# Kernel optimization log

Measured on AMD Instinct MI355X. Metric: run time of the kernel, lower is better.

## Reference

```python
import jax, jax.numpy as jnp
import numpy as np

N_DIMS = 4          # Euclidean GA with metric [1,1,1,1]
NUM_BLADES = 1 << N_DIMS  # 16 blades
B, N_IN, UNITS = 128, 512, 512


def _cayley_table(n_dims: int) -> np.ndarray:
    """Geometric-product Cayley table C[i,j,k] for Euclidean metric (+1,...,+1).

    Blades are indexed by bitmasks over the n basis vectors; e_A * e_B = sign * e_{A^B},
    where sign counts transpositions in the canonical reordering.
    """
    num = 1 << n_dims
    C = np.zeros((num, num, num), dtype=np.float32)
    for a in range(num):
        for b in range(num):
            t, swaps = a >> 1, 0
            while t:
                swaps += bin(t & b).count("1")
                t >>= 1
            C[a, b, a ^ b] = -1.0 if (swaps & 1) else 1.0
    return C


def setup_inputs() -> dict:
    key = jax.random.key(0)
    k1, k2, k3 = jax.random.split(key, 3)
    x = jax.random.normal(k1, (B, N_IN, NUM_BLADES), dtype=jnp.float32)
    w = jax.random.normal(k2, (UNITS, N_IN, NUM_BLADES), dtype=jnp.float32)
    b = jax.random.normal(k3, (UNITS, NUM_BLADES), dtype=jnp.float32)
    cayley = jnp.asarray(_cayley_table(N_DIMS))
    return {"x": x, "w": w, "b": b, "cayley": cayley}


def reference(x, w, b, cayley):
    # geom_prod(x[..., None, n, i], w[u, n, j])[..., u, n, k], summed over n, plus bias:
    # out[b,u,k] = sum_{n,i,j} x[b,n,i] * cayley[i,j,k] * w[u,n,j] + b[u,k]
    out = jnp.einsum("bni,ijk,unj->buk", x, cayley, w)
    return out + b
```

## Files before the change

### kernel.cpp

```cpp
#include <hip/hip_runtime.h>
#include <stdint.h>

typedef unsigned short ushort_t;
typedef __attribute__((ext_vector_type(8))) short short8v;
typedef __attribute__((ext_vector_type(4))) float f32x4;

#define NSPLIT 8

#define AT_ELEMS (16u * 128u * 512u)
#define WT_ELEMS (16u * 512u * 512u)
#define P_OFF_BYTES ((size_t)(AT_ELEMS + WT_ELEMS) * 2u)
#define P_ELEMS ((size_t)NSPLIT * 16 * 128 * 512)
#define WS_NEEDED (P_OFF_BYTES + P_ELEMS * 4u)

__host__ __device__ constexpr int ga_sign_i(int a, int b) {
  int t = a >> 1, sw = 0;
  while (t) {
    int x = t & b;
    while (x) { sw += x & 1; x >>= 1; }
    t >>= 1;
  }
  return (sw & 1) ? -1 : 1;
}

struct SignTab { int s[16][16]; };
constexpr SignTab make_tab() {
  SignTab t{};
  for (int i = 0; i < 16; i++)
    for (int j = 0; j < 16; j++) t.s[i][j] = ga_sign_i(i, j);
  return t;
}
constexpr SignTab STAB = make_tab();

__device__ __forceinline__ ushort_t f2bf(float f) {
  unsigned u = __float_as_uint(f);
  u = (u + 0x7FFFu + ((u >> 16) & 1u)) >> 16;
  return (ushort_t)u;
}

__device__ __forceinline__ short8v neg_bf16x8(short8v v) {
  const short m = (short)0x8000;
  return v ^ (short8v){m, m, m, m, m, m, m, m};
}

#define PREP_XT (128 * 512)
#define PREP_TOT (PREP_XT + 512 * 512)

__global__ __launch_bounds__(256) void prep_kernel(const float* __restrict__ x,
                                                   const float* __restrict__ w,
                                                   ushort_t* __restrict__ At,
                                                   ushort_t* __restrict__ Wt) {
  int tid = blockIdx.x * 256 + threadIdx.x;
  if (tid < PREP_XT) {
    int n = tid & 511, b = tid >> 9;
    const float4* xp = (const float4*)(x + (size_t)tid * 16);
    float v[16];
#pragma unroll
    for (int qq = 0; qq < 4; qq++) {
      float4 t = xp[qq];
      v[qq * 4 + 0] = t.x; v[qq * 4 + 1] = t.y; v[qq * 4 + 2] = t.z; v[qq * 4 + 3] = t.w;
    }
#pragma unroll
    for (int j = 0; j < 16; j++)
      At[((size_t)(j * 128 + b)) * 512 + n] = f2bf(v[j]);
  } else {
    int t = tid - PREP_XT;
    int n = t & 511, u = t >> 9;
    const float4* wp = (const float4*)(w + (size_t)t * 16);
    float v[16];
#pragma unroll
    for (int qq = 0; qq < 4; qq++) {
      float4 tt = wp[qq];
      v[qq * 4 + 0] = tt.x; v[qq * 4 + 1] = tt.y; v[qq * 4 + 2] = tt.z; v[qq * 4 + 3] = tt.w;
    }
#pragma unroll
    for (int j = 0; j < 16; j++)
      Wt[((size_t)(j * 512 + u)) * 512 + n] = f2bf(v[j]);
  }
}

template <int W>
__device__ __forceinline__ void compute_chunk(const char* sm, int lbx,
                                              f32x4 (&acc)[4][2][2]) {
#pragma unroll
  for (int jh = 0; jh < 4; jh++) {
    const int ig = jh ^ W;
    short8v av[4][2], bv[4][2];
#pragma unroll
    for (int il = 0; il < 4; il++)
#pragma unroll
      for (int f = 0; f < 2; f++)
        av[il][f] = *(const short8v*)(sm + ((ig * 4 + il) * 32 + f * 16) * 64 + lbx);
#pragma unroll
    for (int jl = 0; jl < 4; jl++)
#pragma unroll
      for (int g = 0; g < 2; g++)
        bv[jl][g] = *(const short8v*)(sm + 32768 + ((jh * 4 + jl) * 32 + g * 16) * 64 + lbx);
#pragma unroll
    for (int kl = 0; kl < 4; kl++) {
#pragma unroll
      for (int jl = 0; jl < 4; jl++) {
        const int il = jl ^ kl;
        const int i = ig * 4 + il;
        const int j = jh * 4 + jl;
        short8v a0 = av[il][0], a1 = av[il][1];
        if (STAB.s[i][j] < 0) { a0 = neg_bf16x8(a0); a1 = neg_bf16x8(a1); }
        acc[kl][0][0] = __builtin_amdgcn_mfma_f32_16x16x32_bf16(a0, bv[jl][0], acc[kl][0][0], 0, 0, 0);
        acc[kl][0][1] = __builtin_amdgcn_mfma_f32_16x16x32_bf16(a0, bv[jl][1], acc[kl][0][1], 0, 0, 0);
        acc[kl][1][0] = __builtin_amdgcn_mfma_f32_16x16x32_bf16(a1, bv[jl][0], acc[kl][1][0], 0, 0, 0);
        acc[kl][1][1] = __builtin_amdgcn_mfma_f32_16x16x32_bf16(a1, bv[jl][1], acc[kl][1][1], 0, 0, 0);
      }
    }
  }
}

__global__ __launch_bounds__(256, 2) void gemm_kernel(const ushort_t* __restrict__ At,
                                                      const ushort_t* __restrict__ Wt,
                                                      float* __restrict__ P) {
  __shared__ __align__(16) ushort_t smem[32768];

  const int ut = blockIdx.x;
  const int bt = blockIdx.y;
  const int sp = blockIdx.z;
  const int u0 = ut * 32, b0 = bt * 32, n0 = sp * 64;

  const int wv = threadIdx.x >> 6;
  const int lane = threadIdx.x & 63;

  int offX[8], offW[8];
#pragma unroll
  for (int it = 0; it < 8; it++) {
    int slot = it * 256 + wv * 64 + lane;
    int r = slot >> 2, p = slot & 3;
    int q = p ^ (r & 3) ^ ((r >> 2) & 3);
    offX[it] = ((r >> 5) * 128 + (r & 31)) * 512 + q * 8;
    offW[it] = ((r >> 5) * 512 + (r & 31)) * 512 + q * 8;
  }
  const ushort_t* Ax = At + (size_t)b0 * 512 + n0;
  const ushort_t* Wx = Wt + (size_t)u0 * 512 + n0;

  const int la = lane & 15, q = lane >> 4;
  const int lbx = la * 64 + (q ^ (la & 3) ^ ((la >> 2) & 3)) * 16;

  f32x4 acc[4][2][2];
#pragma unroll
  for (int a = 0; a < 4; a++)
#pragma unroll
    for (int f = 0; f < 2; f++)
#pragma unroll
      for (int g = 0; g < 2; g++) acc[a][f][g] = (f32x4){0.f, 0.f, 0.f, 0.f};

  const char* sm = (const char*)smem;

#pragma unroll 1
  for (int kt = 0; kt < 2; kt++) {
#pragma unroll
    for (int it = 0; it < 8; it++)
      __builtin_amdgcn_global_load_lds(
          (const __attribute__((address_space(1))) unsigned int*)(Ax + offX[it] + kt * 32),
          (__attribute__((address_space(3))) unsigned int*)(&smem[(it * 256 + wv * 64) * 8]),
          16, 0, 0);
#pragma unroll
    for (int it = 0; it < 8; it++)
      __builtin_amdgcn_global_load_lds(
          (const __attribute__((address_space(1))) unsigned int*)(Wx + offW[it] + kt * 32),
          (__attribute__((address_space(3))) unsigned int*)(&smem[16384 + (it * 256 + wv * 64) * 8]),
          16, 0, 0);
    __syncthreads();
    switch (wv) {
      case 0: compute_chunk<0>(sm, lbx, acc); break;
      case 1: compute_chunk<1>(sm, lbx, acc); break;
      case 2: compute_chunk<2>(sm, lbx, acc); break;
      default: compute_chunk<3>(sm, lbx, acc); break;
    }
    __syncthreads();
  }

  float* Pb = P + (size_t)sp * 16 * 128 * 512;
#pragma unroll
  for (int kl = 0; kl < 4; kl++) {
    int k = wv * 4 + kl;
#pragma unroll
    for (int f = 0; f < 2; f++)
#pragma unroll
      for (int g = 0; g < 2; g++)
#pragma unroll
        for (int r2 = 0; r2 < 4; r2++) {
          int row = b0 + f * 16 + q * 4 + r2;
          int col = u0 + g * 16 + la;
          Pb[((size_t)(k * 128 + row)) * 512 + col] = acc[kl][f][g][r2];
        }
  }
}

__global__ __launch_bounds__(256) void reduce_kernel(const float* __restrict__ P,
                                                     const float* __restrict__ bias,
                                                     float* __restrict__ out) {
  int t = blockIdx.x * 256 + threadIdx.x;
  int u = t & 511;
  int b = t >> 9;
  float acc[16];
#pragma unroll
  for (int k = 0; k < 16; k++) acc[k] = bias[u * 16 + k];
  for (int s = 0; s < NSPLIT; s++) {
#pragma unroll
    for (int k = 0; k < 16; k++)
      acc[k] += P[((size_t)(s * 16 + k) * 128 + b) * 512 + u];
  }
  float* op = out + ((size_t)(b * 512 + u)) * 16;
#pragma unroll
  for (int qq = 0; qq < 4; qq++)
    ((float4*)op)[qq] = make_float4(acc[qq * 4 + 0], acc[qq * 4 + 1],
                                    acc[qq * 4 + 2], acc[qq * 4 + 3]);
}

__global__ __launch_bounds__(256) void naive_kernel(const float* __restrict__ x,
                                                    const float* __restrict__ w,
                                                    const float* __restrict__ bias,
                                                    float* __restrict__ out) {
  int t = blockIdx.x * 256 + threadIdx.x;
  if (t >= 128 * 512 * 16) return;
  int k = t & 15;
  int u = (t >> 4) & 511;
  int b = t >> 13;
  float sgn[16];
#pragma unroll
  for (int i = 0; i < 16; i++) sgn[i] = (float)ga_sign_i(i, i ^ k);
  float acc = bias[u * 16 + k];
  for (int n = 0; n < 512; n++) {
    const float* xp = x + ((size_t)(b * 512 + n)) * 16;
    const float* wp = w + ((size_t)(u * 512 + n)) * 16;
#pragma unroll
    for (int i = 0; i < 16; i++)
      acc += xp[i] * sgn[i] * wp[i ^ k];
  }
  out[t] = acc;
}

extern "C" void kernel_launch(void* const* d_in, const int* in_sizes, int n_in,
                              void* d_out, int out_size, void* d_ws, size_t ws_size,
                              hipStream_t stream) {
  const float* x    = (const float*)d_in[0];
  const float* w    = (const float*)d_in[1];
  const float* bias = (const float*)d_in[2];
  float* out = (float*)d_out;

  if (ws_size >= WS_NEEDED && d_ws != nullptr) {
    ushort_t* At = (ushort_t*)d_ws;
    ushort_t* Wt = At + AT_ELEMS;
    float* P = (float*)((char*)d_ws + P_OFF_BYTES);

    prep_kernel<<<PREP_TOT / 256, 256, 0, stream>>>(x, w, At, Wt);
    gemm_kernel<<<dim3(16, 4, NSPLIT), 256, 0, stream>>>(At, Wt, P);
    reduce_kernel<<<256, 256, 0, stream>>>(P, bias, out);
  } else {
    naive_kernel<<<(128 * 512 * 16) / 256, 256, 0, stream>>>(x, w, bias, out);
  }
}
```

Baseline: 102.3 us.

## Retile GA GEMM to 16-row batch tiles with fewer K splits and coalesced prep

The GEMM tile becomes 16 batch rows by 32 units with a 128-deep K slice per block, and the K split drops from 8 to 4. This halves the partial-sum buffer that the reduce kernel reads and writes. Each wave now precomputes the negated A fragments once per chunk instead of negating them per MFMA. The prep kernel is rewritten so each thread packs 8 consecutive n values into one 16-byte store, instead of issuing 16 scattered 2-byte stores. In exchange the prep loads become strided, each block does less MFMA work per shared-memory load, and the grid is reshaped.

```diff
diff --git a/kernel.cpp b/kernel.cpp
--- a/kernel.cpp
+++ b/kernel.cpp
@@ -5,7 +5,7 @@
 typedef __attribute__((ext_vector_type(8))) short short8v;
 typedef __attribute__((ext_vector_type(4))) float f32x4;
 
-#define NSPLIT 8
+#define NSPLIT 4
 
 #define AT_ELEMS (16u * 128u * 512u)
 #define WT_ELEMS (16u * 512u * 512u)
@@ -43,8 +43,8 @@
   return v ^ (short8v){m, m, m, m, m, m, m, m};
 }
 
-#define PREP_XT (128 * 512)
-#define PREP_TOT (PREP_XT + 512 * 512)
+#define PREP_XT (16 * 128 * 64)
+#define PREP_TOT (PREP_XT + 16 * 512 * 64)
 
 __global__ __launch_bounds__(256) void prep_kernel(const float* __restrict__ x,
                                                    const float* __restrict__ w,
@@ -52,50 +52,44 @@
                                                    ushort_t* __restrict__ Wt) {
   int tid = blockIdx.x * 256 + threadIdx.x;
   if (tid < PREP_XT) {
-    int n = tid & 511, b = tid >> 9;
-    const float4* xp = (const float4*)(x + (size_t)tid * 16);
-    float v[16];
-#pragma unroll
-    for (int qq = 0; qq < 4; qq++) {
-      float4 t = xp[qq];
-      v[qq * 4 + 0] = t.x; v[qq * 4 + 1] = t.y; v[qq * 4 + 2] = t.z; v[qq * 4 + 3] = t.w;
-    }
-#pragma unroll
-    for (int j = 0; j < 16; j++)
-      At[((size_t)(j * 128 + b)) * 512 + n] = f2bf(v[j]);
+    int n8 = tid & 63;
+    int bj = tid >> 6;
+    int b = bj & 127, j = bj >> 7;
+    ushort_t o[8];
+#pragma unroll
+    for (int r = 0; r < 8; r++)
+      o[r] = f2bf(x[((size_t)(b * 512 + n8 * 8 + r)) * 16 + j]);
+    *(uint4*)(At + ((size_t)(j * 128 + b)) * 512 + n8 * 8) = *(const uint4*)o;
   } else {
     int t = tid - PREP_XT;
-    int n = t & 511, u = t >> 9;
-    const float4* wp = (const float4*)(w + (size_t)t * 16);
-    float v[16];
-#pragma unroll
-    for (int qq = 0; qq < 4; qq++) {
-      float4 tt = wp[qq];
-      v[qq * 4 + 0] = tt.x; v[qq * 4 + 1] = tt.y; v[qq * 4 + 2] = tt.z; v[qq * 4 + 3] = tt.w;
-    }
-#pragma unroll
-    for (int j = 0; j < 16; j++)
-      Wt[((size_t)(j * 512 + u)) * 512 + n] = f2bf(v[j]);
+    int n8 = t & 63;
+    int uj = t >> 6;
+    int u = uj & 511, j = uj >> 9;
+    ushort_t o[8];
+#pragma unroll
+    for (int r = 0; r < 8; r++)
+      o[r] = f2bf(w[((size_t)(u * 512 + n8 * 8 + r)) * 16 + j]);
+    *(uint4*)(Wt + ((size_t)(j * 512 + u)) * 512 + n8 * 8) = *(const uint4*)o;
   }
 }
 
 template <int W>
 __device__ __forceinline__ void compute_chunk(const char* sm, int lbx,
-                                              f32x4 (&acc)[4][2][2]) {
+                                              f32x4 (&acc)[4][2]) {
 #pragma unroll
   for (int jh = 0; jh < 4; jh++) {
     const int ig = jh ^ W;
-    short8v av[4][2], bv[4][2];
-#pragma unroll
-    for (int il = 0; il < 4; il++)
-#pragma unroll
-      for (int f = 0; f < 2; f++)
-        av[il][f] = *(const short8v*)(sm + ((ig * 4 + il) * 32 + f * 16) * 64 + lbx);
+    short8v av[4], avn[4], bv[4][2];
+#pragma unroll
+    for (int il = 0; il < 4; il++) {
+      av[il] = *(const short8v*)(sm + (ig * 4 + il) * 1024 + lbx);
+      avn[il] = neg_bf16x8(av[il]);
+    }
 #pragma unroll
     for (int jl = 0; jl < 4; jl++)
 #pragma unroll
       for (int g = 0; g < 2; g++)
-        bv[jl][g] = *(const short8v*)(sm + 32768 + ((jh * 4 + jl) * 32 + g * 16) * 64 + lbx);
+        bv[jl][g] = *(const short8v*)(sm + 16384 + (jh * 4 + jl) * 2048 + g * 1024 + lbx);
 #pragma unroll
     for (int kl = 0; kl < 4; kl++) {
 #pragma unroll
@@ -103,12 +97,9 @@
         const int il = jl ^ kl;
         const int i = ig * 4 + il;
         const int j = jh * 4 + jl;
-        short8v a0 = av[il][0], a1 = av[il][1];
-        if (STAB.s[i][j] < 0) { a0 = neg_bf16x8(a0); a1 = neg_bf16x8(a1); }
-        acc[kl][0][0] = __builtin_amdgcn_mfma_f32_16x16x32_bf16(a0, bv[jl][0], acc[kl][0][0], 0, 0, 0);
-        acc[kl][0][1] = __builtin_amdgcn_mfma_f32_16x16x32_bf16(a0, bv[jl][1], acc[kl][0][1], 0, 0, 0);
-        acc[kl][1][0] = __builtin_amdgcn_mfma_f32_16x16x32_bf16(a1, bv[jl][0], acc[kl][1][0], 0, 0, 0);
-        acc[kl][1][1] = __builtin_amdgcn_mfma_f32_16x16x32_bf16(a1, bv[jl][1], acc[kl][1][1], 0, 0, 0);
+        const short8v a = (STAB.s[i][j] < 0) ? avn[il] : av[il];
+        acc[kl][0] = __builtin_amdgcn_mfma_f32_16x16x32_bf16(a, bv[jl][0], acc[kl][0], 0, 0, 0);
+        acc[kl][1] = __builtin_amdgcn_mfma_f32_16x16x32_bf16(a, bv[jl][1], acc[kl][1], 0, 0, 0);
       }
     }
   }
@@ -117,23 +108,29 @@
 __global__ __launch_bounds__(256, 2) void gemm_kernel(const ushort_t* __restrict__ At,
                                                       const ushort_t* __restrict__ Wt,
                                                       float* __restrict__ P) {
-  __shared__ __align__(16) ushort_t smem[32768];
+  __shared__ __align__(16) ushort_t smem[24576];
 
   const int ut = blockIdx.x;
   const int bt = blockIdx.y;
   const int sp = blockIdx.z;
-  const int u0 = ut * 32, b0 = bt * 32, n0 = sp * 64;
+  const int u0 = ut * 32, b0 = bt * 16, n0 = sp * 128;
 
   const int wv = threadIdx.x >> 6;
   const int lane = threadIdx.x & 63;
 
-  int offX[8], offW[8];
+  int offX[4], offW[8];
+#pragma unroll
+  for (int it = 0; it < 4; it++) {
+    int slot = it * 256 + wv * 64 + lane;
+    int r = slot >> 2, p = slot & 3;
+    int q = p ^ (r & 3) ^ ((r >> 2) & 3);
+    offX[it] = ((r >> 4) * 128 + (r & 15)) * 512 + q * 8;
+  }
 #pragma unroll
   for (int it = 0; it < 8; it++) {
     int slot = it * 256 + wv * 64 + lane;
     int r = slot >> 2, p = slot & 3;
     int q = p ^ (r & 3) ^ ((r >> 2) & 3);
-    offX[it] = ((r >> 5) * 128 + (r & 31)) * 512 + q * 8;
     offW[it] = ((r >> 5) * 512 + (r & 31)) * 512 + q * 8;
   }
   const ushort_t* Ax = At + (size_t)b0 * 512 + n0;
@@ -142,20 +139,18 @@
   const int la = lane & 15, q = lane >> 4;
   const int lbx = la * 64 + (q ^ (la & 3) ^ ((la >> 2) & 3)) * 16;
 
-  f32x4 acc[4][2][2];
+  f32x4 acc[4][2];
 #pragma unroll
   for (int a = 0; a < 4; a++)
 #pragma unroll
-    for (int f = 0; f < 2; f++)
-#pragma unroll
-      for (int g = 0; g < 2; g++) acc[a][f][g] = (f32x4){0.f, 0.f, 0.f, 0.f};
+    for (int g = 0; g < 2; g++) acc[a][g] = (f32x4){0.f, 0.f, 0.f, 0.f};
 
   const char* sm = (const char*)smem;
 
 #pragma unroll 1
-  for (int kt = 0; kt < 2; kt++) {
-#pragma unroll
-    for (int it = 0; it < 8; it++)
+  for (int kt = 0; kt < 4; kt++) {
+#pragma unroll
+    for (int it = 0; it < 4; it++)
       __builtin_amdgcn_global_load_lds(
           (const __attribute__((address_space(1))) unsigned int*)(Ax + offX[it] + kt * 32),
           (__attribute__((address_space(3))) unsigned int*)(&smem[(it * 256 + wv * 64) * 8]),
@@ -164,7 +159,7 @@
     for (int it = 0; it < 8; it++)
       __builtin_amdgcn_global_load_lds(
           (const __attribute__((address_space(1))) unsigned int*)(Wx + offW[it] + kt * 32),
-          (__attribute__((address_space(3))) unsigned int*)(&smem[16384 + (it * 256 + wv * 64) * 8]),
+          (__attribute__((address_space(3))) unsigned int*)(&smem[8192 + (it * 256 + wv * 64) * 8]),
           16, 0, 0);
     __syncthreads();
     switch (wv) {
@@ -181,15 +176,13 @@
   for (int kl = 0; kl < 4; kl++) {
     int k = wv * 4 + kl;
 #pragma unroll
-    for (int f = 0; f < 2; f++)
-#pragma unroll
-      for (int g = 0; g < 2; g++)
-#pragma unroll
-        for (int r2 = 0; r2 < 4; r2++) {
-          int row = b0 + f * 16 + q * 4 + r2;
-          int col = u0 + g * 16 + la;
-          Pb[((size_t)(k * 128 + row)) * 512 + col] = acc[kl][f][g][r2];
-        }
+    for (int g = 0; g < 2; g++)
+#pragma unroll
+      for (int r2 = 0; r2 < 4; r2++) {
+        int row = b0 + q * 4 + r2;
+        int col = u0 + g * 16 + la;
+        Pb[((size_t)(k * 128 + row)) * 512 + col] = acc[kl][g][r2];
+      }
   }
 }
 
@@ -251,7 +244,7 @@
     float* P = (float*)((char*)d_ws + P_OFF_BYTES);
 
     prep_kernel<<<PREP_TOT / 256, 256, 0, stream>>>(x, w, At, Wt);
-    gemm_kernel<<<dim3(16, 4, NSPLIT), 256, 0, stream>>>(At, Wt, P);
+    gemm_kernel<<<dim3(16, 8, NSPLIT), 256, 0, stream>>>(At, Wt, P);
     reduce_kernel<<<256, 256, 0, stream>>>(P, bias, out);
   } else {
     naive_kernel<<<(128 * 512 * 16) / 256, 256, 0, stream>>>(x, w, bias, out);
```

After: 107.5 us. 5.1% more time.

## Replace split-K partials and reduce kernel with in-block wave reduction

Applied to the files above, without the earlier changes.

Drops the split-K decomposition that wrote fp32 partials to workspace and the separate reduce kernel. Each block now owns a 16x16 (b,u) tile with all 16 output blades. Each wave covers a quarter of the n range and the four waves are summed through shared memory with the bias add fused in. This removes a kernel launch and the large partial-buffer traffic. In exchange it uses 128KB of LDS per block, so only one block fits per CU. The grid also shrinks to 256 blocks and the K loop becomes serial with no overlap between loads and compute.

```diff
diff --git a/kernel.cpp b/kernel.cpp
--- a/kernel.cpp
+++ b/kernel.cpp
@@ -5,13 +5,9 @@
 typedef __attribute__((ext_vector_type(8))) short short8v;
 typedef __attribute__((ext_vector_type(4))) float f32x4;
 
-#define NSPLIT 8
-
 #define AT_ELEMS (16u * 128u * 512u)
 #define WT_ELEMS (16u * 512u * 512u)
-#define P_OFF_BYTES ((size_t)(AT_ELEMS + WT_ELEMS) * 2u)
-#define P_ELEMS ((size_t)NSPLIT * 16 * 128 * 512)
-#define WS_NEEDED (P_OFF_BYTES + P_ELEMS * 4u)
+#define WS_NEEDED ((size_t)(AT_ELEMS + WT_ELEMS) * 2u)
 
 __host__ __device__ constexpr int ga_sign_i(int a, int b) {
   int t = a >> 1, sw = 0;
@@ -79,139 +75,101 @@
   }
 }
 
-template <int W>
-__device__ __forceinline__ void compute_chunk(const char* sm, int lbx,
-                                              f32x4 (&acc)[4][2][2]) {
-#pragma unroll
-  for (int jh = 0; jh < 4; jh++) {
-    const int ig = jh ^ W;
-    short8v av[4][2], bv[4][2];
-#pragma unroll
-    for (int il = 0; il < 4; il++)
-#pragma unroll
-      for (int f = 0; f < 2; f++)
-        av[il][f] = *(const short8v*)(sm + ((ig * 4 + il) * 32 + f * 16) * 64 + lbx);
-#pragma unroll
-    for (int jl = 0; jl < 4; jl++)
-#pragma unroll
-      for (int g = 0; g < 2; g++)
-        bv[jl][g] = *(const short8v*)(sm + 32768 + ((jh * 4 + jl) * 32 + g * 16) * 64 + lbx);
-#pragma unroll
-    for (int kl = 0; kl < 4; kl++) {
-#pragma unroll
-      for (int jl = 0; jl < 4; jl++) {
-        const int il = jl ^ kl;
-        const int i = ig * 4 + il;
-        const int j = jh * 4 + jl;
-        short8v a0 = av[il][0], a1 = av[il][1];
-        if (STAB.s[i][j] < 0) { a0 = neg_bf16x8(a0); a1 = neg_bf16x8(a1); }
-        acc[kl][0][0] = __builtin_amdgcn_mfma_f32_16x16x32_bf16(a0, bv[jl][0], acc[kl][0][0], 0, 0, 0);
-        acc[kl][0][1] = __builtin_amdgcn_mfma_f32_16x16x32_bf16(a0, bv[jl][1], acc[kl][0][1], 0, 0, 0);
-        acc[kl][1][0] = __builtin_amdgcn_mfma_f32_16x16x32_bf16(a1, bv[jl][0], acc[kl][1][0], 0, 0, 0);
-        acc[kl][1][1] = __builtin_amdgcn_mfma_f32_16x16x32_bf16(a1, bv[jl][1], acc[kl][1][1], 0, 0, 0);
-      }
-    }
-  }
-}
-
-__global__ __launch_bounds__(256, 2) void gemm_kernel(const ushort_t* __restrict__ At,
+__global__ __launch_bounds__(256, 1) void gemm_kernel(const ushort_t* __restrict__ At,
                                                       const ushort_t* __restrict__ Wt,
-                                                      float* __restrict__ P) {
-  __shared__ __align__(16) ushort_t smem[32768];
+                                                      const float* __restrict__ bias,
+                                                      float* __restrict__ out) {
+  __shared__ __align__(16) ushort_t smem[65536];
 
   const int ut = blockIdx.x;
   const int bt = blockIdx.y;
-  const int sp = blockIdx.z;
-  const int u0 = ut * 32, b0 = bt * 32, n0 = sp * 64;
-
-  const int wv = threadIdx.x >> 6;
-  const int lane = threadIdx.x & 63;
-
-  int offX[8], offW[8];
-#pragma unroll
-  for (int it = 0; it < 8; it++) {
-    int slot = it * 256 + wv * 64 + lane;
-    int r = slot >> 2, p = slot & 3;
-    int q = p ^ (r & 3) ^ ((r >> 2) & 3);
-    offX[it] = ((r >> 5) * 128 + (r & 31)) * 512 + q * 8;
-    offW[it] = ((r >> 5) * 512 + (r & 31)) * 512 + q * 8;
-  }
-  const ushort_t* Ax = At + (size_t)b0 * 512 + n0;
-  const ushort_t* Wx = Wt + (size_t)u0 * 512 + n0;
-
+  const int u0 = ut * 16, b0 = bt * 16;
+
+  const int tid = threadIdx.x;
+  const int wv = tid >> 6, lane = tid & 63;
   const int la = lane & 15, q = lane >> 4;
-  const int lbx = la * 64 + (q ^ (la & 3) ^ ((la >> 2) & 3)) * 16;
-
-  f32x4 acc[4][2][2];
-#pragma unroll
-  for (int a = 0; a < 4; a++)
-#pragma unroll
-    for (int f = 0; f < 2; f++)
-#pragma unroll
-      for (int g = 0; g < 2; g++) acc[a][f][g] = (f32x4){0.f, 0.f, 0.f, 0.f};
+
+  const int srow = tid >> 4;
+  const int sps = tid & 15;
+  const int sp = sps ^ (srow & 7);
+  const int sc = sp >> 2, sq = sp & 3;
+
+  const ushort_t* AxB = At + (size_t)(b0 + srow) * 512 + sc * 32 + sq * 8;
+  const ushort_t* WxB = Wt + (size_t)(u0 + srow) * 512 + sc * 32 + sq * 8;
+
+  const int pr = wv * 4 + q;
+  const int lbx = la * 256 + ((pr ^ (la & 7)) * 16);
+
+  f32x4 acc[16];
+#pragma unroll
+  for (int k = 0; k < 16; k++) acc[k] = (f32x4){0.f, 0.f, 0.f, 0.f};
 
   const char* sm = (const char*)smem;
 
 #pragma unroll 1
-  for (int kt = 0; kt < 2; kt++) {
-#pragma unroll
-    for (int it = 0; it < 8; it++)
+  for (int kt = 0; kt < 4; kt++) {
+#pragma unroll
+    for (int i = 0; i < 16; i++)
       __builtin_amdgcn_global_load_lds(
-          (const __attribute__((address_space(1))) unsigned int*)(Ax + offX[it] + kt * 32),
-          (__attribute__((address_space(3))) unsigned int*)(&smem[(it * 256 + wv * 64) * 8]),
+          (const __attribute__((address_space(1))) unsigned int*)(AxB + (size_t)i * 65536 + kt * 128),
+          (__attribute__((address_space(3))) unsigned int*)(&smem[(i * 256 + wv * 64) * 8]),
           16, 0, 0);
 #pragma unroll
-    for (int it = 0; it < 8; it++)
+    for (int i = 0; i < 16; i++)
       __builtin_amdgcn_global_load_lds(
-          (const __attribute__((address_space(1))) unsigned int*)(Wx + offW[it] + kt * 32),
-          (__attribute__((address_space(3))) unsigned int*)(&smem[16384 + (it * 256 + wv * 64) * 8]),
+          (const __attribute__((address_space(1))) unsigned int*)(WxB + (size_t)i * 262144 + kt * 128),
+          (__attribute__((address_space(3))) unsigned int*)(&smem[32768 + (i * 256 + wv * 64) * 8]),
           16, 0, 0);
     __syncthreads();
-    switch (wv) {
-      case 0: compute_chunk<0>(sm, lbx, acc); break;
-      case 1: compute_chunk<1>(sm, lbx, acc); break;
-      case 2: compute_chunk<2>(sm, lbx, acc); break;
-      default: compute_chunk<3>(sm, lbx, acc); break;
+
+    short8v av[16], nav[16];
+#pragma unroll
+    for (int i = 0; i < 16; i++) {
+      av[i] = *(const short8v*)(sm + i * 4096 + lbx);
+      nav[i] = neg_bf16x8(av[i]);
+    }
+#pragma unroll
+    for (int j = 0; j < 16; j++) {
+      const short8v bvj = *(const short8v*)(sm + 65536 + j * 4096 + lbx);
+#pragma unroll
+      for (int k = 0; k < 16; k++) {
+        const int i = j ^ k;
+        acc[k] = __builtin_amdgcn_mfma_f32_16x16x32_bf16(
+            (STAB.s[i][j] < 0) ? nav[i] : av[i], bvj, acc[k], 0, 0, 0);
+      }
     }
     __syncthreads();
   }
 
-  float* Pb = P + (size_t)sp * 16 * 128 * 512;
-#pragma unroll
-  for (int kl = 0; kl < 4; kl++) {
-    int k = wv * 4 + kl;
-#pragma unroll
-    for (int f = 0; f < 2; f++)
-#pragma unroll
-      for (int g = 0; g < 2; g++)
-#pragma unroll
-        for (int r2 = 0; r2 < 4; r2++) {
-          int row = b0 + f * 16 + q * 4 + r2;
-          int col = u0 + g * 16 + la;
-          Pb[((size_t)(k * 128 + row)) * 512 + col] = acc[kl][f][g][r2];
-        }
-  }
-}
-
-__global__ __launch_bounds__(256) void reduce_kernel(const float* __restrict__ P,
-                                                     const float* __restrict__ bias,
-                                                     float* __restrict__ out) {
-  int t = blockIdx.x * 256 + threadIdx.x;
-  int u = t & 511;
-  int b = t >> 9;
-  float acc[16];
-#pragma unroll
-  for (int k = 0; k < 16; k++) acc[k] = bias[u * 16 + k];
-  for (int s = 0; s < NSPLIT; s++) {
-#pragma unroll
-    for (int k = 0; k < 16; k++)
-      acc[k] += P[((size_t)(s * 16 + k) * 128 + b) * 512 + u];
-  }
-  float* op = out + ((size_t)(b * 512 + u)) * 16;
-#pragma unroll
-  for (int qq = 0; qq < 4; qq++)
-    ((float4*)op)[qq] = make_float4(acc[qq * 4 + 0], acc[qq * 4 + 1],
-                                    acc[qq * 4 + 2], acc[qq * 4 + 3]);
+  float* red = (float*)smem;
+#pragma unroll
+  for (int g = 0; g < 4; g++) {
+#pragma unroll
+    for (int r2 = 0; r2 < 4; r2++) {
+      float4 v = make_float4(acc[g * 4 + 0][r2], acc[g * 4 + 1][r2],
+                             acc[g * 4 + 2][r2], acc[g * 4 + 3][r2]);
+      int row = q * 4 + r2;
+      *(float4*)&red[(((wv * 16 + row) * 16 + la) << 4) + g * 4] = v;
+    }
+  }
+  __syncthreads();
+
+  const int row = tid >> 4, col = tid & 15;
+  float4 o[4];
+#pragma unroll
+  for (int g = 0; g < 4; g++)
+    o[g] = *(const float4*)&bias[(u0 + col) * 16 + g * 4];
+#pragma unroll
+  for (int w2 = 0; w2 < 4; w2++) {
+#pragma unroll
+    for (int g = 0; g < 4; g++) {
+      float4 v = *(const float4*)&red[(((w2 * 16 + row) * 16 + col) << 4) + g * 4];
+      o[g].x += v.x; o[g].y += v.y; o[g].z += v.z; o[g].w += v.w;
+    }
+  }
+#pragma unroll
+  for (int g = 0; g < 4; g++)
+    *(float4*)&out[((size_t)(b0 + row) * 512 + (u0 + col)) * 16 + g * 4] = o[g];
 }
 
 __global__ __launch_bounds__(256) void naive_kernel(const float* __restrict__ x,
@@ -248,11 +206,9 @@
   if (ws_size >= WS_NEEDED && d_ws != nullptr) {
     ushort_t* At = (ushort_t*)d_ws;
     ushort_t* Wt = At + AT_ELEMS;
-    float* P = (float*)((char*)d_ws + P_OFF_BYTES);
 
     prep_kernel<<<PREP_TOT / 256, 256, 0, stream>>>(x, w, At, Wt);
-    gemm_kernel<<<dim3(16, 4, NSPLIT), 256, 0, stream>>>(At, Wt, P);
-    reduce_kernel<<<256, 256, 0, stream>>>(P, bias, out);
+    gemm_kernel<<<dim3(32, 8), 256, 0, stream>>>(At, Wt, bias, out);
   } else {
     naive_kernel<<<(128 * 512 * 16) / 256, 256, 0, stream>>>(x, w, bias, out);
   }
```

Measured after the change: 94.86 us. 7.3% less time.
